# Kernel tuning notes

Measured on AMD Instinct MI355X. Metric: run time of the kernel, lower is better.

The kernel has to match this reference:

```python
import jax, jax.numpy as jnp
import numpy as np

DECAY = 0.99
EPS = 1e-5
COMMIT = 0.25

def setup_inputs() -> dict:
    key = jax.random.key(0)
    k1, k2 = jax.random.split(key)
    inputs = jax.random.normal(k1, (2, 64, 48, 48, 48), dtype=jnp.float32)
    emb_weight = jax.random.normal(k2, (256, 64), dtype=jnp.float32)
    return {
        "inputs": inputs,
        "emb_weight": emb_weight,
        "ema_cluster_size": jnp.zeros((256,), jnp.float32),
        "ema_w": emb_weight.copy(),  # registered buffer initialized as clone of embedding
    }

def reference(inputs, emb_weight, ema_cluster_size, ema_w):
    B, C, D, H, W = inputs.shape
    K = emb_weight.shape[0]
    # quantize: channel-last flatten [B*D*H*W, C]
    flat_input = jnp.transpose(inputs, (0, 2, 3, 4, 1)).reshape(-1, C)
    # pairwise squared distances via norms + matmul
    distances = ((flat_input ** 2).sum(axis=1, keepdims=True)
                 + (emb_weight ** 2).sum(axis=1)[None, :]
                 - 2.0 * flat_input @ emb_weight.T)  # [N, K]
    encoding_indices = jnp.argmin(distances, axis=1)  # [N]
    # embed: gather codebook rows, reshape to channel-first [B, C, D, H, W]
    quantized = jnp.transpose(emb_weight[encoding_indices].reshape(B, D, H, W, C), (0, 4, 1, 2, 3))
    # EMA codebook update (training branch; one-hot sums expressed as segment reductions)
    encodings_sum = jax.ops.segment_sum(jnp.ones(flat_input.shape[0], jnp.float32), encoding_indices, num_segments=K)
    dw = jax.ops.segment_sum(flat_input, encoding_indices, num_segments=K)  # [K, C]
    new_cluster_size = DECAY * ema_cluster_size + (1.0 - DECAY) * encodings_sum
    n = new_cluster_size.sum()
    weights = (new_cluster_size + EPS) / (n + K * EPS) * n
    new_ema_w = DECAY * ema_w + (1.0 - DECAY) * dw
    new_emb_weight = new_ema_w / weights[:, None]
    # commitment loss (quantized detached) scaled by 10, straight-through estimator
    loss = COMMIT * jnp.mean((jax.lax.stop_gradient(quantized) - inputs) ** 2) * 10.0
    quantized_out = inputs + jax.lax.stop_gradient(quantized - inputs)
    enc_idx = encoding_indices.reshape(B, D, H, W)
    return (quantized_out, loss, enc_idx, encodings_sum, new_emb_weight)
```

## Files before the change

kernel.cpp:

```cpp
#include <hip/hip_runtime.h>
#include <hip/hip_bf16.h>

#define SPA 110592
#define NPOS 221184
#define NELEM 14155776
#define KCODES 256
#define CCH 64
#define NPART 256
#define PPB 864
#define DWBLK 432
#define DWTHR 512
#define EPS_TIE 0.0625f

typedef __attribute__((ext_vector_type(8))) short bf16x8;
typedef __attribute__((ext_vector_type(16))) float f32x16;

__device__ __forceinline__ void bf16split(float v, short& h, short& l) {
    unsigned bits = __builtin_bit_cast(unsigned, v);
    h = (short)(bits >> 16);
    float hf = __builtin_bit_cast(float, bits & 0xFFFF0000u);
    float res = v - hf;
    l = (short)(__builtin_bit_cast(unsigned, res) >> 16);
}

__device__ __forceinline__ float bf16join(short h, short l) {
    float hf = __builtin_bit_cast(float, ((unsigned)(unsigned short)h) << 16);
    float lf = __builtin_bit_cast(float, ((unsigned)(unsigned short)l) << 16);
    return hf + lf;
}

__device__ __forceinline__ float dpack(float d, int k) {
    unsigned bits = (__builtin_bit_cast(unsigned, d) & 0xFFFFFF00u) | (unsigned)k;
    return __builtin_bit_cast(float, bits);
}
__device__ __forceinline__ int dkey(float d) {
    return (int)(__builtin_bit_cast(unsigned, d) & 0xFFu);
}

__device__ __forceinline__ void top2merge(float& m1, float& m2, float o1, float o2) {
    float a = fminf(m1, o1);
    float b = fmaxf(m1, o1);
    m2 = fminf(b, fminf(m2, o2));
    m1 = a;
}

__global__ __launch_bounds__(256) void vq_init(
    const float* __restrict__ emb, float* __restrict__ en2,
    float* __restrict__ dw, float* __restrict__ hist, float* __restrict__ loss,
    float* __restrict__ fragH, float* __restrict__ fragL)
{
    int t = blockIdx.x * 256 + threadIdx.x;
    if (t < CCH * KCODES) dw[t] = 0.f;
    if (t < 2048) {
        int g = t >> 6, lane = t & 63;
        int w = g >> 3, ct = (g >> 2) & 1, j = g & 3;
        int code = w * 64 + ct * 32 + (lane & 31);
        int ch0 = (lane >> 5) * 8 + j * 16;
        const float* er = emb + (code << 6) + ch0;
        bf16x8 hfr, lfr;
#pragma unroll
        for (int jj = 0; jj < 8; ++jj) {
            short hs, ls; bf16split(er[jj], hs, ls);
            hfr[jj] = hs; lfr[jj] = ls;
        }
        ((bf16x8*)fragH)[t] = hfr;
        ((bf16x8*)fragL)[t] = lfr;
    }
    if (t >= 2048 && t < 4096) {
        int t2 = t - 2048;
        int code = t2 >> 3, seg = t2 & 7;
        const float* e = emb + (code << 6) + seg * 8;
        float s = 0.f;
#pragma unroll
        for (int jj = 0; jj < 8; ++jj) s = fmaf(e[jj], e[jj], s);
        s += __shfl_down(s, 4, 64);
        s += __shfl_down(s, 2, 64);
        s += __shfl_down(s, 1, 64);
        if (seg == 0) en2[code] = s;
    }
    if (t < KCODES) hist[t] = 0.f;
    if (t == 0) loss[0] = 0.f;
}

__global__ __launch_bounds__(256, 3) void vq_argmin_mfma(
    const float* __restrict__ in, const float* __restrict__ emb,
    const float* __restrict__ en2, const float* __restrict__ fragH,
    const float* __restrict__ fragL, float* __restrict__ qout,
    float* __restrict__ encout, float* __restrict__ hist,
    float* __restrict__ loss)
{
    __shared__ __align__(16) short xh[8][128][8];
    __shared__ __align__(16) short xl[8][128][8];
    __shared__ float e2s[KCODES];
    __shared__ float pm1[4][128], pm2[4][128];
    __shared__ int   bestkS[128];
    __shared__ float lhist[KCODES];
    __shared__ float lred[4];

    int tid  = threadIdx.x;
    int w    = tid >> 6, lane = tid & 63;
    int hi   = lane >> 5, col = lane & 31;
    int wbase = w * 64;

    int blk = blockIdx.x;
    int b   = (blk >= 864) ? 1 : 0;
    int s0  = (blk - b * 864) * 128;
    const float* xbase = in + b * (CCH * SPA) + s0;

    if (tid < KCODES) { e2s[tid] = en2[tid]; lhist[tid] = 0.f; }

    const bf16x8* fH = (const bf16x8*)fragH;
    const bf16x8* fL = (const bf16x8*)fragL;
    bf16x8 Ah[2][4], Al[2][4];
#pragma unroll
    for (int ct = 0; ct < 2; ++ct)
#pragma unroll
        for (int j = 0; j < 4; ++j) {
            int g = (w * 8 + ct * 4 + j) * 64 + lane;
            Ah[ct][j] = fH[g];
            Al[ct][j] = fL[g];
        }

    {
        int tg = tid >> 7, p = tid & 127;
        const float* xb = xbase + p;
#pragma unroll
        for (int cb = 0; cb < 4; ++cb) {
            int c0 = tg * 32 + cb * 8;
            bf16x8 hfr, lfr;
#pragma unroll
            for (int jj = 0; jj < 8; ++jj) {
                short hs, ls; bf16split(xb[(c0 + jj) * SPA], hs, ls);
                hfr[jj] = hs; lfr[jj] = ls;
            }
            *(bf16x8*)&xh[c0 >> 3][p][0] = hfr;
            *(bf16x8*)&xl[c0 >> 3][p][0] = lfr;
        }
    }
    __syncthreads();

#pragma unroll 1
    for (int pt = 0; pt < 4; ++pt) {
        int pos = pt * 32 + col;
        f32x16 c0, c1;
#pragma unroll
        for (int i = 0; i < 16; ++i) { c0[i] = 0.f; c1[i] = 0.f; }

#pragma unroll
        for (int j = 0; j < 4; ++j) {
            bf16x8 bh = *(const bf16x8*)&xh[j * 2 + hi][pos][0];
            bf16x8 bl = *(const bf16x8*)&xl[j * 2 + hi][pos][0];
            c0 = __builtin_amdgcn_mfma_f32_32x32x16_bf16(Ah[0][j], bh, c0, 0, 0, 0);
            c1 = __builtin_amdgcn_mfma_f32_32x32x16_bf16(Ah[1][j], bh, c1, 0, 0, 0);
            c0 = __builtin_amdgcn_mfma_f32_32x32x16_bf16(Ah[0][j], bl, c0, 0, 0, 0);
            c1 = __builtin_amdgcn_mfma_f32_32x32x16_bf16(Ah[1][j], bl, c1, 0, 0, 0);
            c0 = __builtin_amdgcn_mfma_f32_32x32x16_bf16(Al[0][j], bh, c0, 0, 0, 0);
            c1 = __builtin_amdgcn_mfma_f32_32x32x16_bf16(Al[1][j], bh, c1, 0, 0, 0);
        }

        float m1 = 1e30f, m2 = 1e30f;
#pragma unroll
        for (int ct = 0; ct < 2; ++ct) {
#pragma unroll
            for (int r = 0; r < 16; ++r) {
                int kc  = wbase + ct * 32 + (r & 3) + 8 * (r >> 2) + 4 * hi;
                float d = dpack(fmaf(-2.f, (ct ? c1[r] : c0[r]), e2s[kc]), kc);
                float lo  = fminf(d, m1);
                float hi2 = fmaxf(d, m1);
                m2 = fminf(hi2, m2);
                m1 = lo;
            }
        }
        top2merge(m1, m2, __shfl_xor(m1, 32, 64), __shfl_xor(m2, 32, 64));
        if (hi == 0) { pm1[w][pos] = m1; pm2[w][pos] = m2; }
    }
    __syncthreads();

    if (tid < 128) {
        int p = tid;
        float M1 = pm1[0][p], M2 = pm2[0][p];
#pragma unroll
        for (int ww = 1; ww < 4; ++ww)
            top2merge(M1, M2, pm1[ww][p], pm2[ww][p]);
        int K1 = dkey(M1), K2 = dkey(M2);
        int bk = K1;
        if (M2 <= M1 + EPS_TIE) {
            int ka = min(K1, K2), kb = max(K1, K2);
            const float* xb2 = xbase + p;
            const float* ea  = emb + (ka << 6);
            const float* eb2 = emb + (kb << 6);
            float da = 0.f, db = 0.f;
#pragma unroll 4
            for (int c = 0; c < CCH; ++c) {
                float xv = xb2[c * SPA];
                da = fmaf(xv, ea[c], da);
                db = fmaf(xv, eb2[c], db);
            }
            float Da = e2s[ka] - 2.f * da;
            float Db = e2s[kb] - 2.f * db;
            bk = (Db < Da) ? kb : ka;
        }
        bestkS[p] = bk;
        encout[b * SPA + s0 + p] = (float)bk;
        atomicAdd(&lhist[bk], 1.0f);
    }
    __syncthreads();

    {
        int tg = tid >> 7, p = tid & 127;
        int k = bestkS[p];
        const float* ee = emb + (k << 6) + tg * 32;
        float* qp = qout + b * (CCH * SPA) + s0 + p;
        float lsum = 0.f;
#pragma unroll
        for (int cb = 0; cb < 4; ++cb) {
            int oct = tg * 4 + cb;
            bf16x8 hfr = *(const bf16x8*)&xh[oct][p][0];
            bf16x8 lfr = *(const bf16x8*)&xl[oct][p][0];
#pragma unroll
            for (int jj = 0; jj < 8; ++jj) {
                float xv = bf16join(hfr[jj], lfr[jj]);
                float q  = ee[cb * 8 + jj];
                float d  = q - xv;
                lsum = fmaf(d, d, lsum);
                qp[(tg * 32 + cb * 8 + jj) * SPA] = q;
            }
        }
        for (int off = 32; off > 0; off >>= 1) lsum += __shfl_down(lsum, off, 64);
        if (lane == 0) lred[w] = lsum;
    }
    __syncthreads();
    if (tid == 0)
        unsafeAtomicAdd(loss, (lred[0] + lred[1] + lred[2] + lred[3]) * (2.5f / 14155776.f));
    if (tid < KCODES && lhist[tid] != 0.f)
        unsafeAtomicAdd(&hist[tid], lhist[tid]);
}

__global__ __launch_bounds__(512) void vq_dw_part(
    const float* __restrict__ in, const float* __restrict__ encout,
    float* __restrict__ partial)
{
    __shared__ float l[CCH * KCODES];
    int tid = threadIdx.x;
#pragma unroll
    for (int i = tid; i < CCH * KCODES; i += 512) l[i] = 0.f;
    __syncthreads();

    int base = blockIdx.x * PPB;
    int b    = (blockIdx.x >= 128) ? 1 : 0;
    {
        int n = base + tid;
        int s = n - b * SPA;
        int k = (int)encout[n];
        const float* xp = in + b * (CCH * SPA) + s;
#pragma unroll
        for (int c = 0; c < CCH; ++c)
            atomicAdd(&l[(c << 8) + (k ^ (c & 31))], xp[c * SPA]);
    }
    if (tid < PPB - 512) {
        int n = base + 512 + tid;
        int s = n - b * SPA;
        int k = (int)encout[n];
        const float* xp = in + b * (CCH * SPA) + s;
#pragma unroll
        for (int c = 0; c < CCH; ++c)
            atomicAdd(&l[(c << 8) + (k ^ (c & 31))], xp[c * SPA]);
    }
    __syncthreads();

    float* pp = partial + (size_t)blockIdx.x * (CCH * KCODES);
#pragma unroll
    for (int i = tid; i < CCH * KCODES; i += 512) {
        int k2 = i >> 6, c = i & 63;
        pp[i] = l[(c << 8) + (k2 ^ (c & 31))];
    }
}

__global__ __launch_bounds__(256) void vq_dw_reduce(
    const float* __restrict__ partial, float* __restrict__ dw)
{
    __shared__ float acc[4][64];
    int t = threadIdx.x, lane6 = t & 63, tsub = t >> 6;
    int i = blockIdx.x * 64 + lane6;
    float s = 0.f;
    for (int p = tsub * 64; p < tsub * 64 + 64; ++p)
        s += partial[(size_t)p * (CCH * KCODES) + i];
    acc[tsub][lane6] = s;
    __syncthreads();
    if (tsub == 0)
        dw[i] = (acc[0][lane6] + acc[1][lane6]) + (acc[2][lane6] + acc[3][lane6]);
}

__global__ __launch_bounds__(DWTHR) void vq_dw_atomic(
    const float* __restrict__ in, const float* __restrict__ encout,
    float* __restrict__ dw)
{
    __shared__ float l[CCH * KCODES];
    int tid = threadIdx.x;
    for (int i = tid; i < CCH * KCODES; i += DWTHR) l[i] = 0.f;
    __syncthreads();
    int n = blockIdx.x * DWTHR + tid;
    int b = (n >= SPA) ? 1 : 0;
    int s = n - b * SPA;
    int k = (int)encout[n];
    const float* xp = in + b * (CCH * SPA) + s;
#pragma unroll
    for (int c = 0; c < CCH; ++c)
        atomicAdd(&l[(c << 8) + (k ^ (c & 31))], xp[c * SPA]);
    __syncthreads();
    for (int i = tid; i < CCH * KCODES; i += DWTHR) {
        int k2 = i >> 6, c = i & 63;
        unsafeAtomicAdd(&dw[i], l[(c << 8) + (k2 ^ (c & 31))]);
    }
}

__global__ __launch_bounds__(1024) void vq_ema(
    const float* __restrict__ csize, const float* __restrict__ emaw,
    const float* __restrict__ hist, const float* __restrict__ dw,
    float* __restrict__ embo)
{
    __shared__ float red[KCODES];
    __shared__ float wsm[KCODES];
    int t = threadIdx.x;
    float ncs = 0.f;
    if (t < KCODES) { ncs = 0.99f * csize[t] + 0.01f * hist[t]; red[t] = ncs; }
    __syncthreads();
    for (int off = 128; off > 0; off >>= 1) {
        if (t < off) red[t] += red[t + off];
        __syncthreads();
    }
    float nsum = red[0];
    if (t < KCODES) wsm[t] = (ncs + 1e-5f) / (nsum + 256.f * 1e-5f) * nsum;
    __syncthreads();
    for (int i = t; i < CCH * KCODES; i += 1024) {
        float nw = fmaf(0.01f, dw[i], 0.99f * emaw[i]);
        embo[i] = nw / wsm[i >> 6];
    }
}

extern "C" void kernel_launch(void* const* d_in, const int* in_sizes, int n_in,
                              void* d_out, int out_size, void* d_ws, size_t ws_size,
                              hipStream_t stream)
{
    const float* in   = (const float*)d_in[0];
    const float* emb  = (const float*)d_in[1];
    const float* cs   = (const float*)d_in[2];
    const float* emaw = (const float*)d_in[3];

    float* out  = (float*)d_out;
    float* qout = out;
    float* loss = out + NELEM;
    float* enc  = loss + 1;
    float* hist = enc + NPOS;
    float* embo = hist + KCODES;

    float* en2     = (float*)d_ws;
    float* dw      = en2 + KCODES;
    float* fragH   = dw + CCH * KCODES;
    float* fragL   = fragH + 8192;
    float* partial = fragL + 8192;

    size_t need = (size_t)(KCODES + CCH * KCODES + 16384) * 4
                + (size_t)NPART * CCH * KCODES * 4;
    bool use_part = (ws_size >= need);

    vq_init<<<dim3(64), dim3(256), 0, stream>>>(emb, en2, dw, hist, loss, fragH, fragL);
    vq_argmin_mfma<<<dim3(1728), dim3(256), 0, stream>>>(in, emb, en2, fragH, fragL,
                                                         qout, enc, hist, loss);
    if (use_part) {
        vq_dw_part<<<dim3(NPART), dim3(512), 0, stream>>>(in, enc, partial);
        vq_dw_reduce<<<dim3(256), dim3(256), 0, stream>>>(partial, dw);
    } else {
        vq_dw_atomic<<<dim3(DWBLK), dim3(DWTHR), 0, stream>>>(in, enc, dw);
    }
    vq_ema<<<dim3(1), dim3(1024), 0, stream>>>(cs, emaw, hist, dw, embo);
}
```

Measured before the change: 274.5 us.

## Compute codebook segment sums with one-hot MFMA instead of LDS atomics

```diff
diff --git a/kernel.cpp b/kernel.cpp
--- a/kernel.cpp
+++ b/kernel.cpp
@@ -6,8 +6,8 @@
 #define NELEM 14155776
 #define KCODES 256
 #define CCH 64
-#define NPART 256
-#define PPB 864
+#define DWG 432
+#define DWCHUNK 128
 #define DWBLK 432
 #define DWTHR 512
 #define EPS_TIE 0.0625f
@@ -236,59 +236,105 @@
         unsafeAtomicAdd(&hist[tid], lhist[tid]);
 }
 
-__global__ __launch_bounds__(512) void vq_dw_part(
+__global__ __launch_bounds__(512, 2) void vq_dw_mfma(
     const float* __restrict__ in, const float* __restrict__ encout,
     float* __restrict__ partial)
 {
-    __shared__ float l[CCH * KCODES];
+    __shared__ __align__(16) short xTh[2][16][64][8];
+    __shared__ __align__(16) short xTl[2][16][64][8];
+    __shared__ int encS[2][DWCHUNK];
+
     int tid = threadIdx.x;
-#pragma unroll
-    for (int i = tid; i < CCH * KCODES; i += 512) l[i] = 0.f;
-    __syncthreads();
-
-    int base = blockIdx.x * PPB;
-    int b    = (blockIdx.x >= 128) ? 1 : 0;
-    {
-        int n = base + tid;
-        int s = n - b * SPA;
-        int k = (int)encout[n];
-        const float* xp = in + b * (CCH * SPA) + s;
-#pragma unroll
-        for (int c = 0; c < CCH; ++c)
-            atomicAdd(&l[(c << 8) + (k ^ (c & 31))], xp[c * SPA]);
-    }
-    if (tid < PPB - 512) {
-        int n = base + 512 + tid;
-        int s = n - b * SPA;
-        int k = (int)encout[n];
-        const float* xp = in + b * (CCH * SPA) + s;
-#pragma unroll
-        for (int c = 0; c < CCH; ++c)
-            atomicAdd(&l[(c << 8) + (k ^ (c & 31))], xp[c * SPA]);
-    }
-    __syncthreads();
-
-    float* pp = partial + (size_t)blockIdx.x * (CCH * KCODES);
-#pragma unroll
-    for (int i = tid; i < CCH * KCODES; i += 512) {
-        int k2 = i >> 6, c = i & 63;
-        pp[i] = l[(c << 8) + (k2 ^ (c & 31))];
+    int w = tid >> 6, lane = tid & 63;
+    int blk = blockIdx.x;
+    int b = (blk >= 216) ? 1 : 0;
+    int sbase = blk * 512 - b * SPA;
+    const float* xb = in + (size_t)b * (CCH * SPA);
+
+    f32x16 acc0, acc1;
+#pragma unroll
+    for (int i = 0; i < 16; ++i) { acc0[i] = 0.f; acc1[i] = 0.f; }
+
+    auto stage = [&](int buf, int t) {
+        int base = sbase + t * DWCHUNK;
+#pragma unroll
+        for (int half = 0; half < 2; ++half) {
+            int it = half * 512 + tid;
+            int c = it >> 4, oct = it & 15;
+            const float* src = xb + (size_t)c * SPA + base + oct * 8;
+            float4 v0 = *(const float4*)src;
+            float4 v1 = *(const float4*)(src + 4);
+            float vv[8] = {v0.x, v0.y, v0.z, v0.w, v1.x, v1.y, v1.z, v1.w};
+            bf16x8 hfr, lfr;
+#pragma unroll
+            for (int jj = 0; jj < 8; ++jj) {
+                short hs, ls; bf16split(vv[jj], hs, ls);
+                hfr[jj] = hs; lfr[jj] = ls;
+            }
+            int cx = c ^ (oct & 7);
+            *(bf16x8*)&xTh[buf][oct][cx][0] = hfr;
+            *(bf16x8*)&xTl[buf][oct][cx][0] = lfr;
+        }
+        if (tid < DWCHUNK)
+            encS[buf][tid] = (int)encout[blk * 512 + t * DWCHUNK + tid];
+    };
+
+    auto compute = [&](int buf) {
+        int mycode = w * 32 + (lane & 31);
+#pragma unroll
+        for (int ks = 0; ks < 8; ++ks) {
+            int kbase = ks * 16 + (lane >> 5) * 8;
+            int po = kbase >> 3;
+            const int* ep = &encS[buf][kbase];
+            bf16x8 afr;
+#pragma unroll
+            for (int jj = 0; jj < 8; ++jj)
+                afr[jj] = (ep[jj] == mycode) ? (short)0x3F80 : (short)0;
+            int kx = po & 7;
+            int j0 = (lane & 31) ^ kx;
+            bf16x8 bh0 = *(const bf16x8*)&xTh[buf][po][j0][0];
+            bf16x8 bl0 = *(const bf16x8*)&xTl[buf][po][j0][0];
+            bf16x8 bh1 = *(const bf16x8*)&xTh[buf][po][32 + j0][0];
+            bf16x8 bl1 = *(const bf16x8*)&xTl[buf][po][32 + j0][0];
+            acc0 = __builtin_amdgcn_mfma_f32_32x32x16_bf16(afr, bh0, acc0, 0, 0, 0);
+            acc0 = __builtin_amdgcn_mfma_f32_32x32x16_bf16(afr, bl0, acc0, 0, 0, 0);
+            acc1 = __builtin_amdgcn_mfma_f32_32x32x16_bf16(afr, bh1, acc1, 0, 0, 0);
+            acc1 = __builtin_amdgcn_mfma_f32_32x32x16_bf16(afr, bl1, acc1, 0, 0, 0);
+        }
+    };
+
+    stage(0, 0);
+    __syncthreads();
+#pragma unroll 1
+    for (int t = 0; t < 4; ++t) {
+        if (t < 3) stage((t + 1) & 1, t + 1);
+        compute(t & 1);
+        __syncthreads();
+    }
+
+    float* pp = partial + (size_t)blk * (CCH * KCODES);
+#pragma unroll
+    for (int r = 0; r < 16; ++r) {
+        int code = w * 32 + (r & 3) + 8 * (r >> 2) + 4 * (lane >> 5);
+        int ch = lane & 31;
+        pp[code * 64 + ch]      = acc0[r];
+        pp[code * 64 + 32 + ch] = acc1[r];
     }
 }
 
 __global__ __launch_bounds__(256) void vq_dw_reduce(
     const float* __restrict__ partial, float* __restrict__ dw)
 {
-    __shared__ float acc[4][64];
-    int t = threadIdx.x, lane6 = t & 63, tsub = t >> 6;
-    int i = blockIdx.x * 64 + lane6;
-    float s = 0.f;
-    for (int p = tsub * 64; p < tsub * 64 + 64; ++p)
-        s += partial[(size_t)p * (CCH * KCODES) + i];
-    acc[tsub][lane6] = s;
-    __syncthreads();
-    if (tsub == 0)
-        dw[i] = (acc[0][lane6] + acc[1][lane6]) + (acc[2][lane6] + acc[3][lane6]);
+    int i = blockIdx.x * 256 + threadIdx.x;
+    float s0 = 0.f, s1 = 0.f, s2 = 0.f, s3 = 0.f;
+#pragma unroll 2
+    for (int p = 0; p < DWG; p += 4) {
+        s0 += partial[(size_t)(p + 0) * (CCH * KCODES) + i];
+        s1 += partial[(size_t)(p + 1) * (CCH * KCODES) + i];
+        s2 += partial[(size_t)(p + 2) * (CCH * KCODES) + i];
+        s3 += partial[(size_t)(p + 3) * (CCH * KCODES) + i];
+    }
+    dw[i] = (s0 + s1) + (s2 + s3);
 }
 
 __global__ __launch_bounds__(DWTHR) void vq_dw_atomic(
@@ -361,15 +407,15 @@
     float* partial = fragL + 8192;
 
     size_t need = (size_t)(KCODES + CCH * KCODES + 16384) * 4
-                + (size_t)NPART * CCH * KCODES * 4;
+                + (size_t)DWG * CCH * KCODES * 4;
     bool use_part = (ws_size >= need);
 
     vq_init<<<dim3(64), dim3(256), 0, stream>>>(emb, en2, dw, hist, loss, fragH, fragL);
     vq_argmin_mfma<<<dim3(1728), dim3(256), 0, stream>>>(in, emb, en2, fragH, fragL,
                                                          qout, enc, hist, loss);
     if (use_part) {
-        vq_dw_part<<<dim3(NPART), dim3(512), 0, stream>>>(in, enc, partial);
-        vq_dw_reduce<<<dim3(256), dim3(256), 0, stream>>>(partial, dw);
+        vq_dw_mfma<<<dim3(DWG), dim3(512), 0, stream>>>(in, enc, partial);
+        vq_dw_reduce<<<dim3(64), dim3(256), 0, stream>>>(partial, dw);
     } else {
         vq_dw_atomic<<<dim3(DWBLK), dim3(DWTHR), 0, stream>>>(in, enc, dw);
     }
```

Measured after the change: 238.1 us. 1.15x faster.
